# Performance work log

Measured on AMD Instinct MI355X. Metric: run time of the kernel, lower is better.

The kernel has to match this reference:

```python
import jax, jax.numpy as jnp
import numpy as np

D_MODEL = 1024
N_HEADS = 16
D_H = D_MODEL // N_HEADS
B, T = 4, 2048
NEG_INF = jnp.finfo(jnp.float32).min


def setup_inputs() -> dict:
    key = jax.random.key(0)
    ks = jax.random.split(key, 9)
    s = 1.0 / np.sqrt(D_MODEL)
    inp = {
        "x": jax.random.normal(ks[0], (B, T, D_MODEL), dtype=jnp.float32),
        "pad_mask": jnp.zeros((B, T), dtype=bool),
        "Wq": jax.random.uniform(ks[1], (D_MODEL, D_MODEL), jnp.float32, -s, s),
        "bq": jax.random.uniform(ks[2], (D_MODEL,), jnp.float32, -s, s),
        "Wk": jax.random.uniform(ks[3], (D_MODEL, D_MODEL), jnp.float32, -s, s),
        "bk": jax.random.uniform(ks[4], (D_MODEL,), jnp.float32, -s, s),
        "Wv": jax.random.uniform(ks[5], (D_MODEL, D_MODEL), jnp.float32, -s, s),
        "bv": jax.random.uniform(ks[6], (D_MODEL,), jnp.float32, -s, s),
        "Wo": jax.random.uniform(ks[7], (D_MODEL, D_MODEL), jnp.float32, -s, s),
        "bo": jax.random.uniform(ks[8], (D_MODEL,), jnp.float32, -s, s),
    }
    return inp


def reference(x, pad_mask, Wq, bq, Wk, bk, Wv, bv, Wo, bo):
    b, t, _ = x.shape
    # torch Linear: y = x @ W.T + b
    def proj(W, bias):
        y = jnp.einsum("btd,ed->bte", x, W) + bias
        return y.reshape(b, t, N_HEADS, D_H).transpose(0, 2, 1, 3)  # (B,H,T,d_h)

    Q, K, V = proj(Wq, bq), proj(Wk, bk), proj(Wv, bv)
    S = jnp.einsum("bhqd,bhkd->bhqk", Q, K) / jnp.sqrt(jnp.float32(D_H))
    causal = jnp.triu(jnp.ones((t, t), dtype=bool), k=1)[None, None]
    S = jnp.where(causal, NEG_INF, S)
    S = jnp.where(pad_mask[:, None, None, :], NEG_INF, S)
    A = jax.nn.softmax(S, axis=-1)
    Y = jnp.einsum("bhqk,bhkd->bhqd", A, V)
    Y = Y.transpose(0, 2, 1, 3).reshape(b, t, D_MODEL)
    O = jnp.einsum("btd,ed->bte", Y, Wo) + bo
    return O
```

## Files before the change

kernel.cpp:

```cpp
#include <hip/hip_runtime.h>
#include <stdint.h>
#include <stddef.h>

#define Tq 2048
#define DM 1024

typedef unsigned short u16;
typedef __bf16 bf16x8 __attribute__((ext_vector_type(8)));
typedef float f32x4 __attribute__((ext_vector_type(4)));
typedef unsigned short u16x8 __attribute__((ext_vector_type(8)));

__device__ __forceinline__ float bf2f(u16 h) {
    union { unsigned int u; float f; } c; c.u = ((unsigned int)h) << 16; return c.f;
}
__device__ __forceinline__ u16 f2bf(float f) {
    union { float f; unsigned int u; } c; c.f = f;
    unsigned int u = c.u;
    return (u16)((u + 0x7fffu + ((u >> 16) & 1u)) >> 16);
}

#define GLD(gp, lp) __builtin_amdgcn_global_load_lds(                                  \
        (const __attribute__((address_space(1))) void*)(gp),                           \
        (__attribute__((address_space(3))) void*)(lp), 16, 0, 0)

__device__ __forceinline__ int sniff_fp32(const u16* xs) {
    const int lane = threadIdx.x & 63;
    const u16 u = xs[lane];
    const int e = (u >> 7) & 0xFF;
    unsigned long long m = __ballot(e >= 160);
    return __popcll(m) >= 4;
}

__device__ __forceinline__ void cvt_body(const void* src, u16* dst, int i0, int fmt) {
    if (fmt) {
        const float* s = (const float*)src;
        float4 a = *(const float4*)(s + i0);
        float4 b = *(const float4*)(s + i0 + 4);
        u16x8 o;
        o[0] = f2bf(a.x); o[1] = f2bf(a.y); o[2] = f2bf(a.z); o[3] = f2bf(a.w);
        o[4] = f2bf(b.x); o[5] = f2bf(b.y); o[6] = f2bf(b.z); o[7] = f2bf(b.w);
        *(u16x8*)(dst + i0) = o;
    } else {
        *(u16x8*)(dst + i0) = *(const u16x8*)((const u16*)src + i0);
    }
}

__global__ void cvt_tensor(const void* __restrict__ src, u16* __restrict__ dst, int n,
                           const u16* __restrict__ xs, int* flag, int writeflag) {
    const int fmt = sniff_fp32(xs);
    if (writeflag && blockIdx.x == 0 && threadIdx.x == 0) *flag = fmt;
    const int i0 = (blockIdx.x * 256 + threadIdx.x) * 8;
    if (i0 >= n) return;
    cvt_body(src, dst, i0, fmt);
}

__global__ void cvt_w4b(const void* s0, const void* s1, const void* s2, const void* s3,
                        const void* t0, const void* t1, const void* t2, const void* t3,
                        u16* __restrict__ dstW, float* __restrict__ dstB,
                        const u16* __restrict__ xs) {
    const int fmt = sniff_fp32(xs);
    const int wsel = blockIdx.y;
    const void* s = (wsel == 0) ? s0 : (wsel == 1) ? s1 : (wsel == 2) ? s2 : s3;
    u16* d = dstW + (size_t)wsel * (DM * DM);
    const int i0 = (blockIdx.x * 256 + threadIdx.x) * 8;
    cvt_body(s, d, i0, fmt);
    if (blockIdx.x == 0) {
        const void* bs = (wsel == 0) ? t0 : (wsel == 1) ? t1 : (wsel == 2) ? t2 : t3;
        float* db = dstB + (size_t)wsel * DM;
        const int j0 = threadIdx.x * 4;
        if (fmt) {
            *(float4*)(db + j0) = *(const float4*)((const float*)bs + j0);
        } else {
            const u16* ss = (const u16*)bs;
            db[j0+0] = bf2f(ss[j0+0]); db[j0+1] = bf2f(ss[j0+1]);
            db[j0+2] = bf2f(ss[j0+2]); db[j0+3] = bf2f(ss[j0+3]);
        }
    }
}

__global__ __launch_bounds__(256, 2) void gemm_bt(
    const u16* __restrict__ A,
    const u16* __restrict__ W0, const u16* __restrict__ W1, const u16* __restrict__ W2,
    const float* __restrict__ b0, const float* __restrict__ b1, const float* __restrict__ b2,
    u16* o0, u16* o1, u16* o2,
    const int* __restrict__ flag, int mode)
{
    __shared__ u16 Alds[128 * 64];
    __shared__ u16 Blds[128 * 64];

    const int K = DM;
    const int i = blockIdx.x;
    const int j = blockIdx.y;
    const int which = (mode == 0) ? (j >> 3) : 0;
    const u16* W      = (which == 0) ? W0 : (which == 1) ? W1 : W2;
    const float* bias = (which == 0) ? b0 : (which == 1) ? b1 : b2;
    u16* out          = (which == 0) ? o0 : (which == 1) ? o1 : o2;
    const int jn = (mode == 0) ? (j & 7) : j;
    const int m0 = i * 128, n0 = jn * 128;
    const int ofmt = (mode == 1) ? *flag : 0;

    const int tid = threadIdx.x;
    const int w = tid >> 6, lane = tid & 63;
    const int l4 = lane & 15, quad = lane >> 4;
    const int wrow = w >> 1, wcol = w & 1;

    f32x4 acc[4][4] = {};

    for (int k0 = 0; k0 < K; k0 += 64) {
        __syncthreads();
#pragma unroll
        for (int c = 0; c < 4; ++c) {
            const int u   = w * 1024 + c * 4096;
            const int off = u + lane * 16;
            const int row = off >> 7;
            const int col = (off & 127) >> 1;
            GLD(A + (size_t)(m0 + row) * K + k0 + col, (char*)Alds + u);
            GLD(W + (size_t)(n0 + row) * K + k0 + col, (char*)Blds + u);
        }
        __syncthreads();
#pragma unroll
        for (int c = 0; c < 2; ++c) {
            bf16x8 af[4], bfr[4];
#pragma unroll
            for (int r = 0; r < 4; ++r)
                af[r] = *(const bf16x8*)&Alds[(wrow*64 + r*16 + l4) * 64 + c*32 + quad*8];
#pragma unroll
            for (int n = 0; n < 4; ++n)
                bfr[n] = *(const bf16x8*)&Blds[(wcol*64 + n*16 + l4) * 64 + c*32 + quad*8];
#pragma unroll
            for (int r = 0; r < 4; ++r)
#pragma unroll
                for (int n = 0; n < 4; ++n)
                    acc[r][n] = __builtin_amdgcn_mfma_f32_16x16x32_bf16(af[r], bfr[n], acc[r][n], 0, 0, 0);
        }
    }

#pragma unroll
    for (int n = 0; n < 4; ++n) {
        const int col = n0 + wcol*64 + n*16 + l4;
        const float bv = bias[col];
#pragma unroll
        for (int r = 0; r < 4; ++r) {
            const int mb = m0 + wrow*64 + r*16 + quad*4;
#pragma unroll
            for (int reg = 0; reg < 4; ++reg) {
                const int m = mb + reg;
                const float val = acc[r][n][reg] + bv;
                if (mode == 0) {
                    const int b = m >> 11, t = m & 2047;
                    const int h = col >> 6, d = col & 63;
                    out[(size_t)((b*16 + h) * 2048 + t) * 64 + d] = f2bf(val);
                } else if (ofmt) {
                    ((float*)out)[(size_t)m * DM + col] = val;
                } else {
                    out[(size_t)m * DM + col] = f2bf(val);
                }
            }
        }
    }
}

#define GSTR 72
__global__ __launch_bounds__(256, 4) void vtrans(
    const u16* __restrict__ Vb, u16* __restrict__ VT)
{
    __shared__ u16 T[64 * GSTR];
    const int t0 = blockIdx.x * 64;
    const int bh = blockIdx.y;
    const u16* src = Vb + (size_t)bh * (Tq * 64);
    u16* dst       = VT + (size_t)bh * (64 * Tq);

    const int tid  = threadIdx.x;
    const int trow = tid >> 2;
    const int c16  = (tid & 3) * 16;
    {
        u16x8 a = *(const u16x8*)&src[(size_t)(t0 + trow) * 64 + c16];
        u16x8 b = *(const u16x8*)&src[(size_t)(t0 + trow) * 64 + c16 + 8];
        const int s  = (trow + (trow >> 3)) & 7;
        const int g0 = c16 >> 3;
        *(u16x8*)&T[trow * GSTR + ((g0 ^ s) << 3)]       = a;
        *(u16x8*)&T[trow * GSTR + (((g0 + 1) ^ s) << 3)] = b;
    }
    __syncthreads();
    const int d  = tid >> 2;
    const int j0 = (tid & 3) * 16;
    u16x8 o0, o1;
#pragma unroll
    for (int e = 0; e < 8; ++e) {
        const int ta = j0 + e, tb = j0 + 8 + e;
        const int sa = (ta + (ta >> 3)) & 7, sb = (tb + (tb >> 3)) & 7;
        o0[e] = T[ta * GSTR + ((((d >> 3) ^ sa) << 3) | (d & 7))];
        o1[e] = T[tb * GSTR + ((((d >> 3) ^ sb) << 3) | (d & 7))];
    }
    *(u16x8*)&dst[(size_t)d * Tq + t0 + j0]     = o0;
    *(u16x8*)&dst[(size_t)d * Tq + t0 + j0 + 8] = o1;
}

#define LSTR 72

__global__ __launch_bounds__(256, 2) void attn4(
    const u16* __restrict__ Qb, const u16* __restrict__ Kb, const u16* __restrict__ VT,
    const unsigned char* __restrict__ pad,
    u16* __restrict__ Y)
{
    __shared__ u16 Klds[64 * LSTR];
    __shared__ u16 Vtl [64 * LSTR];
    __shared__ u16 Pl  [4][64 * LSTR];
    __shared__ unsigned char padl[64];

    const int nb = blockIdx.y;
    const int bh = blockIdx.x;
    const int b = bh >> 4, h = bh & 15;
    const u16* Qp  = Qb + (size_t)bh * (Tq * 64);
    const u16* Kp  = Kb + (size_t)bh * (Tq * 64);
    const u16* VTp = VT + (size_t)bh * (64 * Tq);

    const int tid = threadIdx.x;
    const int w = tid >> 6, lane = tid & 63;
    const int l4 = lane & 15, quad = lane >> 4;

    const int qt[4] = { nb, nb + 8, 23 - nb, 31 - nb };

    bf16x8 qf[4][2];
#pragma unroll
    for (int g = 0; g < 4; ++g) {
        const u16* r = Qp + (size_t)(qt[g] * 64 + w * 16 + l4) * 64 + quad * 8;
        qf[g][0] = *(const bf16x8*)r;
        qf[g][1] = *(const bf16x8*)(r + 32);
    }

    f32x4 o[4][4] = {};
    float l[4][4] = {};

    const int srow = tid >> 2;
    const int sc   = (tid & 3) * 16;

    u16x8 kr0, kr1, vr0, vr1; unsigned char pr = 0;
    {
        const u16* kg = Kp + (size_t)srow * 64 + sc;
        kr0 = *(const u16x8*)kg; kr1 = *(const u16x8*)(kg + 8);
        const u16* vg = VTp + (size_t)srow * Tq + sc;
        vr0 = *(const u16x8*)vg; vr1 = *(const u16x8*)(vg + 8);
        if (tid < 64) pr = pad[(size_t)b * Tq + tid];
    }

    const float SC = 0.18033688011112042f;
    const int ktmax = qt[3];

    for (int kt = 0; kt <= ktmax; ++kt) {
        const int k0 = kt * 64;
        __syncthreads();
        *(u16x8*)&Klds[srow * LSTR + sc]     = kr0;
        *(u16x8*)&Klds[srow * LSTR + sc + 8] = kr1;
        *(u16x8*)&Vtl [srow * LSTR + sc]     = vr0;
        *(u16x8*)&Vtl [srow * LSTR + sc + 8] = vr1;
        if (tid < 64) padl[tid] = pr;
        __syncthreads();
        if (kt < ktmax) {
            const u16* kg = Kp + (size_t)(k0 + 64 + srow) * 64 + sc;
            kr0 = *(const u16x8*)kg; kr1 = *(const u16x8*)(kg + 8);
            const u16* vg = VTp + (size_t)srow * Tq + k0 + 64 + sc;
            vr0 = *(const u16x8*)vg; vr1 = *(const u16x8*)(vg + 8);
            if (tid < 64) pr = pad[(size_t)b * Tq + k0 + 64 + tid];
        }

        bool pm[4];
#pragma unroll
        for (int n = 0; n < 4; ++n) pm[n] = (padl[n * 16 + l4] != 0);

        bf16x8 kf[2][4];
#pragma unroll
        for (int c = 0; c < 2; ++c)
#pragma unroll
            for (int n = 0; n < 4; ++n)
                kf[c][n] = *(const bf16x8*)&Klds[(n * 16 + l4) * LSTR + c * 32 + quad * 8];

#pragma unroll
        for (int g = 0; g < 4; ++g) {
            if (kt > qt[g]) continue;
            f32x4 sacc[4] = {};
            __builtin_amdgcn_s_setprio(1);
#pragma unroll
            for (int c = 0; c < 2; ++c)
#pragma unroll
                for (int n = 0; n < 4; ++n)
                    sacc[n] = __builtin_amdgcn_mfma_f32_16x16x32_bf16(qf[g][c], kf[c][n], sacc[n], 0, 0, 0);
            __builtin_amdgcn_s_setprio(0);
            const int qr = qt[g] * 64 + w * 16 + quad * 4;
            u16* Pg = &Pl[g][0];
#pragma unroll
            for (int r = 0; r < 4; ++r) {
                float rs = 0.f;
#pragma unroll
                for (int n = 0; n < 4; ++n) {
                    const int kgi = k0 + n * 16 + l4;
                    const bool msk = (kgi > qr + r) || pm[n];
                    const float p = msk ? 0.0f : exp2f(sacc[n][r] * SC);
                    rs += p;
                    *(__bf16*)&Pg[(w * 16 + quad * 4 + r) * LSTR + n * 16 + l4] = (__bf16)p;
                }
                l[g][r] += rs;
            }
        }

        bf16x8 vf[2][4];
#pragma unroll
        for (int c = 0; c < 2; ++c)
#pragma unroll
            for (int t = 0; t < 4; ++t)
                vf[c][t] = *(const bf16x8*)&Vtl[(t * 16 + l4) * LSTR + c * 32 + quad * 8];

#pragma unroll
        for (int g = 0; g < 4; ++g) {
            if (kt > qt[g]) continue;
            __builtin_amdgcn_s_setprio(1);
#pragma unroll
            for (int c = 0; c < 2; ++c) {
                bf16x8 pf = *(const bf16x8*)&Pl[g][(w * 16 + l4) * LSTR + c * 32 + quad * 8];
#pragma unroll
                for (int t = 0; t < 4; ++t)
                    o[g][t] = __builtin_amdgcn_mfma_f32_16x16x32_bf16(pf, vf[c][t], o[g][t], 0, 0, 0);
            }
            __builtin_amdgcn_s_setprio(0);
        }
    }

#pragma unroll
    for (int g = 0; g < 4; ++g)
#pragma unroll
        for (int r = 0; r < 4; ++r)
#pragma unroll
            for (int s = 1; s < 16; s <<= 1)
                l[g][r] += __shfl_xor(l[g][r], s);

#pragma unroll
    for (int g = 0; g < 4; ++g)
#pragma unroll
        for (int r = 0; r < 4; ++r) {
            const float inv = 1.0f / l[g][r];
            u16* y = Y + (size_t)(b * Tq + (qt[g] * 64 + w * 16 + quad * 4 + r)) * DM + h * 64;
#pragma unroll
            for (int t = 0; t < 4; ++t)
                *(__bf16*)&y[t * 16 + l4] = (__bf16)(o[g][t][r] * inv);
        }
}

extern "C" void kernel_launch(void* const* d_in, const int* in_sizes, int n_in,
                              void* d_out, int out_size, void* d_ws, size_t ws_size,
                              hipStream_t stream) {
    const void* x  = d_in[0];
    const unsigned char* pad = (const unsigned char*)d_in[1];
    const void* Wq = d_in[2];
    const void* bq = d_in[3];
    const void* Wk = d_in[4];
    const void* bk = d_in[5];
    const void* Wv = d_in[6];
    const void* bv = d_in[7];
    const void* Wo = d_in[8];
    const void* bo = d_in[9];
    const u16* xs = (const u16*)x;

    const size_t NEL = (size_t)8192 * 1024;
    const size_t WEL = (size_t)1024 * 1024;

    int* flag   = (int*)d_ws;
    u16* base16 = (u16*)((char*)d_ws + 256);
    u16* xc     = base16;
    u16* Wc     = base16 + NEL;
    float* bf_  = (float*)(base16 + NEL + 4*WEL);
    u16* Qb     = (u16*)(bf_ + 4096);
    u16* Kb     = Qb + NEL;
    u16* Vb     = Kb + NEL;
    u16* VT     = Vb + NEL;
    u16* Yb     = xc;

    cvt_tensor<<<dim3((int)(NEL/2048)), 256, 0, stream>>>(x, xc, (int)NEL, xs, flag, 1);
    cvt_w4b<<<dim3(512, 4), 256, 0, stream>>>(Wq, Wk, Wv, Wo, bq, bk, bv, bo, Wc, bf_, xs);

    gemm_bt<<<dim3(64, 24), 256, 0, stream>>>(xc, Wc, Wc + WEL, Wc + 2*WEL,
                                              bf_, bf_ + 1024, bf_ + 2048,
                                              Qb, Kb, Vb, flag, 0);
    vtrans<<<dim3(32, 64), 256, 0, stream>>>(Vb, VT);
    attn4<<<dim3(64, 8), 256, 0, stream>>>(Qb, Kb, VT, pad, Yb);
    gemm_bt<<<dim3(64, 8), 256, 0, stream>>>(Yb, Wc + 3*WEL, Wc + 3*WEL, Wc + 3*WEL,
                                             bf_ + 3072, bf_ + 3072, bf_ + 3072,
                                             (u16*)d_out, nullptr, nullptr, flag, 1);
}
```

Measured before the change: 295.5 us.

## Write V transposed from projection GEMM epilogue; skip masking on interior attention tiles

The QKV GEMM epilogue now writes the V projection directly in a (b,h,d,t) transposed layout with packed 4-element stores, which removes the separate vtrans kernel launch and its extra read and write of V. Separately, the attention kernel takes the causal and padding mask path only on diagonal tiles or when any key in the tile is padded, and uses a mask-free exp loop elsewhere. This removes a launch and a full V round trip plus per-element mask compares, but the transposed stores from the GEMM are strided by 2048 elements and may coalesce poorly.

```diff
diff --git a/kernel.cpp b/kernel.cpp
--- a/kernel.cpp
+++ b/kernel.cpp
@@ -9,6 +9,7 @@
 typedef __bf16 bf16x8 __attribute__((ext_vector_type(8)));
 typedef float f32x4 __attribute__((ext_vector_type(4)));
 typedef unsigned short u16x8 __attribute__((ext_vector_type(8)));
+typedef unsigned short u16x4 __attribute__((ext_vector_type(4)));
 
 __device__ __forceinline__ float bf2f(u16 h) {
     union { unsigned int u; float f; } c; c.u = ((unsigned int)h) << 16; return c.f;
@@ -142,58 +143,31 @@
 #pragma unroll
         for (int r = 0; r < 4; ++r) {
             const int mb = m0 + wrow*64 + r*16 + quad*4;
-#pragma unroll
-            for (int reg = 0; reg < 4; ++reg) {
-                const int m = mb + reg;
-                const float val = acc[r][n][reg] + bv;
-                if (mode == 0) {
-                    const int b = m >> 11, t = m & 2047;
-                    const int h = col >> 6, d = col & 63;
-                    out[(size_t)((b*16 + h) * 2048 + t) * 64 + d] = f2bf(val);
-                } else if (ofmt) {
-                    ((float*)out)[(size_t)m * DM + col] = val;
-                } else {
-                    out[(size_t)m * DM + col] = f2bf(val);
+            if (mode == 0 && which == 2) {
+                const int b = mb >> 11, t0 = mb & 2047;
+                const int h = col >> 6, d = col & 63;
+                u16x4 pk;
+#pragma unroll
+                for (int reg = 0; reg < 4; ++reg) pk[reg] = f2bf(acc[r][n][reg] + bv);
+                *(u16x4*)&out[((size_t)(b*16 + h) * 64 + d) * 2048 + t0] = pk;
+            } else {
+#pragma unroll
+                for (int reg = 0; reg < 4; ++reg) {
+                    const int m = mb + reg;
+                    const float val = acc[r][n][reg] + bv;
+                    if (mode == 0) {
+                        const int b = m >> 11, t = m & 2047;
+                        const int h = col >> 6, d = col & 63;
+                        out[(size_t)((b*16 + h) * 2048 + t) * 64 + d] = f2bf(val);
+                    } else if (ofmt) {
+                        ((float*)out)[(size_t)m * DM + col] = val;
+                    } else {
+                        out[(size_t)m * DM + col] = f2bf(val);
+                    }
                 }
             }
         }
     }
-}
-
-#define GSTR 72
-__global__ __launch_bounds__(256, 4) void vtrans(
-    const u16* __restrict__ Vb, u16* __restrict__ VT)
-{
-    __shared__ u16 T[64 * GSTR];
-    const int t0 = blockIdx.x * 64;
-    const int bh = blockIdx.y;
-    const u16* src = Vb + (size_t)bh * (Tq * 64);
-    u16* dst       = VT + (size_t)bh * (64 * Tq);
-
-    const int tid  = threadIdx.x;
-    const int trow = tid >> 2;
-    const int c16  = (tid & 3) * 16;
-    {
-        u16x8 a = *(const u16x8*)&src[(size_t)(t0 + trow) * 64 + c16];
-        u16x8 b = *(const u16x8*)&src[(size_t)(t0 + trow) * 64 + c16 + 8];
-        const int s  = (trow + (trow >> 3)) & 7;
-        const int g0 = c16 >> 3;
-        *(u16x8*)&T[trow * GSTR + ((g0 ^ s) << 3)]       = a;
-        *(u16x8*)&T[trow * GSTR + (((g0 + 1) ^ s) << 3)] = b;
-    }
-    __syncthreads();
-    const int d  = tid >> 2;
-    const int j0 = (tid & 3) * 16;
-    u16x8 o0, o1;
-#pragma unroll
-    for (int e = 0; e < 8; ++e) {
-        const int ta = j0 + e, tb = j0 + 8 + e;
-        const int sa = (ta + (ta >> 3)) & 7, sb = (tb + (tb >> 3)) & 7;
-        o0[e] = T[ta * GSTR + ((((d >> 3) ^ sa) << 3) | (d & 7))];
-        o1[e] = T[tb * GSTR + ((((d >> 3) ^ sb) << 3) | (d & 7))];
-    }
-    *(u16x8*)&dst[(size_t)d * Tq + t0 + j0]     = o0;
-    *(u16x8*)&dst[(size_t)d * Tq + t0 + j0 + 8] = o1;
 }
 
 #define LSTR 72
@@ -264,9 +238,7 @@
             if (tid < 64) pr = pad[(size_t)b * Tq + k0 + 64 + tid];
         }
 
-        bool pm[4];
-#pragma unroll
-        for (int n = 0; n < 4; ++n) pm[n] = (padl[n * 16 + l4] != 0);
+        const bool anypad = __any((int)(padl[lane] != 0));
 
         bf16x8 kf[2][4];
 #pragma unroll
@@ -286,20 +258,37 @@
                 for (int n = 0; n < 4; ++n)
                     sacc[n] = __builtin_amdgcn_mfma_f32_16x16x32_bf16(qf[g][c], kf[c][n], sacc[n], 0, 0, 0);
             __builtin_amdgcn_s_setprio(0);
-            const int qr = qt[g] * 64 + w * 16 + quad * 4;
             u16* Pg = &Pl[g][0];
-#pragma unroll
-            for (int r = 0; r < 4; ++r) {
-                float rs = 0.f;
-#pragma unroll
-                for (int n = 0; n < 4; ++n) {
-                    const int kgi = k0 + n * 16 + l4;
-                    const bool msk = (kgi > qr + r) || pm[n];
-                    const float p = msk ? 0.0f : exp2f(sacc[n][r] * SC);
-                    rs += p;
-                    *(__bf16*)&Pg[(w * 16 + quad * 4 + r) * LSTR + n * 16 + l4] = (__bf16)p;
+            if (kt == qt[g] || anypad) {
+                bool pm[4];
+#pragma unroll
+                for (int n = 0; n < 4; ++n) pm[n] = (padl[n * 16 + l4] != 0);
+                const int qr = qt[g] * 64 + w * 16 + quad * 4;
+#pragma unroll
+                for (int r = 0; r < 4; ++r) {
+                    float rs = 0.f;
+#pragma unroll
+                    for (int n = 0; n < 4; ++n) {
+                        const int kgi = k0 + n * 16 + l4;
+                        const bool msk = (kgi > qr + r) || pm[n];
+                        const float p = msk ? 0.0f : exp2f(sacc[n][r] * SC);
+                        rs += p;
+                        *(__bf16*)&Pg[(w * 16 + quad * 4 + r) * LSTR + n * 16 + l4] = (__bf16)p;
+                    }
+                    l[g][r] += rs;
                 }
-                l[g][r] += rs;
+            } else {
+#pragma unroll
+                for (int r = 0; r < 4; ++r) {
+                    float rs = 0.f;
+#pragma unroll
+                    for (int n = 0; n < 4; ++n) {
+                        const float p = exp2f(sacc[n][r] * SC);
+                        rs += p;
+                        *(__bf16*)&Pg[(w * 16 + quad * 4 + r) * LSTR + n * 16 + l4] = (__bf16)p;
+                    }
+                    l[g][r] += rs;
+                }
             }
         }
 
@@ -370,8 +359,7 @@
     float* bf_  = (float*)(base16 + NEL + 4*WEL);
     u16* Qb     = (u16*)(bf_ + 4096);
     u16* Kb     = Qb + NEL;
-    u16* Vb     = Kb + NEL;
-    u16* VT     = Vb + NEL;
+    u16* VT     = Kb + NEL;
     u16* Yb     = xc;
 
     cvt_tensor<<<dim3((int)(NEL/2048)), 256, 0, stream>>>(x, xc, (int)NEL, xs, flag, 1);
@@ -379,8 +367,7 @@
 
     gemm_bt<<<dim3(64, 24), 256, 0, stream>>>(xc, Wc, Wc + WEL, Wc + 2*WEL,
                                               bf_, bf_ + 1024, bf_ + 2048,
-                                              Qb, Kb, Vb, flag, 0);
-    vtrans<<<dim3(32, 64), 256, 0, stream>>>(Vb, VT);
+                                              Qb, Kb, VT, flag, 0);
     attn4<<<dim3(64, 8), 256, 0, stream>>>(Qb, Kb, VT, pad, Yb);
     gemm_bt<<<dim3(64, 8), 256, 0, stream>>>(Yb, Wc + 3*WEL, Wc + 3*WEL, Wc + 3*WEL,
                                              bf_ + 3072, bf_ + 3072, bf_ + 3072,
```

After: 282.0 us. -4.6%, faster.
